# Optimization experiments

Hardware: AMD Instinct MI355X
Metric: run time of the kernel (lower is better)

The kernel has to match this reference:

```python
import jax, jax.numpy as jnp
import numpy as np

# D4 Daubechies filter taps (same filter replicated across all channels)
D4 = jnp.array([0.4829629131445341, 0.8365163037378079, 0.2241438680420134, -0.1294095225512604], dtype=jnp.float32)
N_SCALES = 11
SPARSE_DILATIONS = (512, 1024)


def setup_inputs() -> dict:
    key = jax.random.key(0)
    ks = jax.random.split(key, 12)
    B, N, D, H = 4, 4096, 1024, 16
    s = 0.02
    return {
        "x": jax.random.normal(ks[0], (B, N, D), dtype=jnp.float32),
        "Wqkv": jax.random.normal(ks[1], (D, 3 * D), dtype=jnp.float32) * s,
        "bqkv": jnp.zeros((3 * D,), dtype=jnp.float32),
        "Wout": jax.random.normal(ks[2], (D, D), dtype=jnp.float32) * s,
        "bout": jnp.zeros((D,), dtype=jnp.float32),
        "Wgate": jax.random.normal(ks[3], (D, D), dtype=jnp.float32) * s,
        "bgate": jnp.full((D,), 2.0, dtype=jnp.float32),  # nn.init.constant_(bias, 2.0)
        "scale_gain": jax.random.normal(ks[4], (N_SCALES, H), dtype=jnp.float32) * 0.1,
        "skip_w": jnp.full((len(SPARSE_DILATIONS),), -4.0, dtype=jnp.float32)
                  + jax.random.normal(ks[5], (len(SPARSE_DILATIONS),), dtype=jnp.float32) * 0.1,
        "coupling": jnp.eye(H, dtype=jnp.float32)
                    + 0.01 * jax.random.normal(ks[6], (H, H), dtype=jnp.float32),
    }


def _shift_right(t, s, N):
    """Causal shift along seq axis (axis=2): out[i] = t[i-s], zeros for i < s."""
    if s == 0:
        return t
    return jnp.pad(t, ((0, 0), (0, 0), (s, 0), (0, 0)))[:, :, :N, :]


def reference(x, Wqkv, bqkv, Wout, bout, Wgate, bgate, scale_gain, skip_w, coupling):
    B, N, D = x.shape
    H = scale_gain.shape[1]
    HD = D // H

    qkv = x @ Wqkv + bqkv                       # [B, N, 3D]
    q, k, v = jnp.split(qkv, 3, axis=-1)

    def to_heads(t):
        return t.reshape(B, N, H, HD).transpose(0, 2, 1, 3)  # [B, H, N, HD]

    q, k, v = to_heads(q), to_heads(k), to_heads(v)

    k_mag = jnp.linalg.norm(k, axis=-1, keepdims=True)       # [B, H, N, 1]
    field = v * k_mag                                        # [B, H, N, HD]

    # --- 11-scale causal D4 dilated depthwise conv pyramid ---
    # Depthwise conv with identical filter on every channel == weighted sum of
    # causally shifted copies: y[n] = sum_t D4[t] * field[n - (3-t)*d]
    gains = jax.nn.softmax(scale_gain, axis=0)               # [S, H]
    acc = jnp.zeros_like(field)
    for j in range(scale_gain.shape[0]):
        d = 1 << j
        y = sum(D4[t] * _shift_right(field, (3 - t) * d, N) for t in range(4))
        acc = acc + gains[j][None, :, None, None] * y
    field = acc

    # --- sparse long-distance causal skips (1-tap copies at d=512, 1024) ---
    sw = jax.nn.sigmoid(skip_w)
    skip = sum(sw[i] * _shift_right(field, d, N) for i, d in enumerate(SPARSE_DILATIONS))
    field = field + skip

    # --- gated field coupling across heads ---
    coup = jax.nn.softmax(coupling, axis=-1)                 # [H, H]
    field = jnp.einsum('ij,bjnd->bind', coup, field)

    q_flat = q.transpose(0, 2, 1, 3).reshape(B, N, D)
    gate = jax.nn.sigmoid(q_flat @ Wgate + bgate)
    gathered = field.transpose(0, 2, 1, 3).reshape(B, N, D)
    out = (gathered * gate) @ Wout + bout                    # dropout = identity (eval)
    return out
```

## Files before the change

### kernel.cpp

```cpp
#include <hip/hip_runtime.h>
#include <hip/hip_bf16.h>
#include <math.h>

#define BB 4
#define NSEQ 4096
#define DD 1024
#define HH 16
#define HD 64
#define MROWS (BB * NSEQ)

typedef __attribute__((ext_vector_type(8))) short short8;
typedef float v4f __attribute__((ext_vector_type(4)));
typedef unsigned short u16;

typedef __attribute__((address_space(1))) const void gconst_void;
typedef __attribute__((address_space(3))) void lds_void_t;

__device__ __constant__ int SHIFTS[24] = {0,1,2,3,4,6,8,12,16,24,32,48,64,96,128,192,256,384,512,768,1024,1536,2048,3072};

__device__ inline u16 f2bf(float f) {
    unsigned u = __float_as_uint(f);
    unsigned r = u + 0x7fffu + ((u >> 16) & 1u);
    return (u16)(r >> 16);
}
__device__ inline float bf2f(u16 h) {
    return __uint_as_float(((unsigned)h) << 16);
}
__device__ inline void gl2lds16(const u16* g, u16* l) {
    __builtin_amdgcn_global_load_lds((gconst_void*)g, (lds_void_t*)l, 16, 0, 0);
}

__device__ inline void tcast_dev(const float* __restrict__ W, long ldw, u16* __restrict__ WT, long ldt,
                                 int bx, int by, int tx, int ty, float (*tile)[33]) {
    long xg = (long)bx * 32 + tx;
    long y0 = (long)by * 32;
    for (int r = 0; r < 32; r += 8)
        tile[ty + r][tx] = W[(y0 + ty + r) * ldw + xg];
    __syncthreads();
    for (int r = 0; r < 32; r += 8)
        WT[((long)bx * 32 + ty + r) * ldt + y0 + tx] = f2bf(tile[tx][ty + r]);
}

__global__ __launch_bounds__(256) void prep_data_kernel(
    const float* __restrict__ x, const float* __restrict__ Wqkv,
    const float* __restrict__ Wgate, const float* __restrict__ Wout,
    const float* __restrict__ bqkv, const float* __restrict__ bgate,
    const float* __restrict__ scale_gain, const float* __restrict__ skip_w,
    const float* __restrict__ coupling,
    u16* __restrict__ xb, u16* __restrict__ WkvT, u16* __restrict__ WgateT,
    u16* __restrict__ WoutT, u16* __restrict__ WqC,
    float* __restrict__ bfuse, float* __restrict__ coefTab,
    float* __restrict__ coupS, float* __restrict__ swbuf) {
    __shared__ float tile[32][33];
    __shared__ float part[4][64];
    const int bid = blockIdx.x;
    const int t = threadIdx.x;
    const int tx = t & 31, ty = t >> 5;

    if (bid < 8192) {
        long i = ((long)bid * 256 + t) * 8;
        float4 f0 = *(const float4*)&x[i];
        float4 f1 = *(const float4*)&x[i + 4];
        u16 o[8];
        o[0] = f2bf(f0.x); o[1] = f2bf(f0.y); o[2] = f2bf(f0.z); o[3] = f2bf(f0.w);
        o[4] = f2bf(f1.x); o[5] = f2bf(f1.y); o[6] = f2bf(f1.z); o[7] = f2bf(f1.w);
        *(uint4*)&xb[i] = *(uint4*)o;
    } else if (bid < 10240) {
        int r = bid - 8192;
        tcast_dev(Wqkv + 1024, 3072, WkvT, 1024, r & 63, r >> 6, tx, ty, tile);
    } else if (bid < 11264) {
        int r = bid - 10240;
        tcast_dev(Wgate, 1024, WgateT, 1024, r & 31, r >> 5, tx, ty, tile);
    } else if (bid < 12288) {
        int r = bid - 11264;
        tcast_dev(Wout, 1024, WoutT, 1024, r & 31, r >> 5, tx, ty, tile);
    } else if (bid < 13312) {
        int r = bid - 12288;
        long i = ((long)r * 256 + t) * 4;
        int row = (int)(i >> 10);
        int col = (int)(i & 1023);
        float4 f = *(const float4*)&Wqkv[(long)row * 3072 + col];
        ushort4 o;
        o.x = f2bf(f.x); o.y = f2bf(f.y); o.z = f2bf(f.z); o.w = f2bf(f.w);
        *(ushort4*)&WqC[i] = o;
    } else if (bid < 13328) {
        int r = bid - 13312;
        int nloc = t & 63, strip = t >> 6;
        int n = r * 64 + nloc;
        float s = 0.f;
        for (int j = strip * 256; j < strip * 256 + 256; j++)
            s += bqkv[j] * Wgate[(long)j * 1024 + n];
        part[strip][nloc] = s;
        __syncthreads();
        if (strip == 0)
            bfuse[n] = bgate[n] + part[0][nloc] + part[1][nloc] + part[2][nloc] + part[3][nloc];
    } else {
        const float D4T[4] = {0.4829629131445341f, 0.8365163037378079f, 0.2241438680420134f, -0.1294095225512604f};
        if (t < 2) swbuf[t] = 1.0f / (1.0f + expf(-skip_w[t]));
        if (t < 16) {
            float m = -1e30f;
            for (int j = 0; j < 16; j++) m = fmaxf(m, coupling[t * 16 + j]);
            float s = 0.f, e[16];
            for (int j = 0; j < 16; j++) { e[j] = expf(coupling[t * 16 + j] - m); s += e[j]; }
            for (int j = 0; j < 16; j++) coupS[t * 16 + j] = e[j] / s;
            float g[11];
            m = -1e30f;
            for (int j = 0; j < 11; j++) m = fmaxf(m, scale_gain[j * 16 + t]);
            s = 0.f;
            for (int j = 0; j < 11; j++) { g[j] = expf(scale_gain[j * 16 + t] - m); s += g[j]; }
            for (int j = 0; j < 11; j++) g[j] /= s;
            float cf[24];
            for (int i = 0; i < 24; i++) cf[i] = 0.f;
            for (int j = 0; j < 11; j++) {
                int d = 1 << j;
                for (int tt = 0; tt < 4; tt++) {
                    int sh = (3 - tt) * d;
                    for (int i = 0; i < 24; i++) {
                        if (SHIFTS[i] == sh) { cf[i] += g[j] * D4T[tt]; break; }
                    }
                }
            }
            for (int i = 0; i < 24; i++) coefTab[t * 24 + i] = cf[i];
        }
    }
}

__global__ __launch_bounds__(256) void gemm64(const u16* __restrict__ A, long lda,
                                              const u16* __restrict__ BT, long ldb, int K,
                                              u16* __restrict__ C, long ldc) {
    __shared__ u16 As[64 * 32];
    __shared__ u16 Bs[64 * 32];
    const int tid = threadIdx.x;
    const int wv = tid >> 6, lane = tid & 63;
    const int wm = wv >> 1, wn = wv & 1;
    const int lrow = lane & 15, kq = lane >> 4;
    const long m0 = (long)blockIdx.y * 64, n0 = (long)blockIdx.x * 64;

    const int srow = wv * 16 + (lane >> 2);
    const int scol = ((lane & 3) ^ ((lane >> 3) & 3)) * 8;
    const u16* gA = A + (m0 + srow) * lda + scol;
    const u16* gB = BT + (n0 + srow) * ldb + scol;
    u16* la = &As[wv * 16 * 32];
    u16* lb = &Bs[wv * 16 * 32];

    const int acol = (kq ^ ((lrow >> 1) & 3)) * 8;
    v4f acc[2][2];
#pragma unroll
    for (int i = 0; i < 2; i++)
#pragma unroll
        for (int j = 0; j < 2; j++) acc[i][j] = (v4f){0.f, 0.f, 0.f, 0.f};

    for (int k0 = 0; k0 < K; k0 += 32) {
        gl2lds16(gA + k0, la);
        gl2lds16(gB + k0, lb);
        __syncthreads();
        short8 af[2], bf[2];
#pragma unroll
        for (int i = 0; i < 2; i++) af[i] = *(const short8*)&As[(wm * 32 + i * 16 + lrow) * 32 + acol];
#pragma unroll
        for (int j = 0; j < 2; j++) bf[j] = *(const short8*)&Bs[(wn * 32 + j * 16 + lrow) * 32 + acol];
#pragma unroll
        for (int im = 0; im < 2; im++)
#pragma unroll
            for (int in = 0; in < 2; in++)
                acc[im][in] = __builtin_amdgcn_mfma_f32_16x16x32_bf16(af[im], bf[in], acc[im][in], 0, 0, 0);
        __syncthreads();
    }
#pragma unroll
    for (int im = 0; im < 2; im++) {
#pragma unroll
        for (int in = 0; in < 2; in++) {
            long row = m0 + wm * 32 + im * 16 + kq * 4;
            long col = n0 + wn * 32 + in * 16 + lrow;
#pragma unroll
            for (int i = 0; i < 4; i++)
                C[(row + i) * ldc + col] = f2bf(acc[im][in][i]);
        }
    }
}

#define WAITV(N) asm volatile("s_waitcnt vmcnt(" #N ")" ::: "memory")

template <int CMODE>
__global__ __launch_bounds__(512, 2) void gemm256(const u16* __restrict__ A, long lda,
                                                  const u16* __restrict__ BT, long ldb, int K,
                                                  const float* __restrict__ bias,
                                                  const float* __restrict__ bias2,
                                                  void* __restrict__ C0, void* __restrict__ C1,
                                                  long ldc, float* __restrict__ kmagOut) {
    __shared__ u16 smem[4 * 2 * 8192];
    const int tid = threadIdx.x;
    const int wv = tid >> 6, lane = tid & 63;
    const int wm = wv >> 2, wn = wv & 3;
    const int lrow = lane & 15, kq = lane >> 4;

    const int nwg = gridDim.x * gridDim.y;
    const int lbid = blockIdx.y * gridDim.x + blockIdx.x;
    const int swz = (lbid & 7) * (nwg >> 3) + (lbid >> 3);
    const int bx = swz % gridDim.x, by = swz / gridDim.x;
    const long m0 = (long)by * 256, n0 = (long)bx * 256;

    const int srow = wv * 32 + (lane >> 2);
    const int scol = ((lane & 3) ^ ((lane >> 3) & 3)) * 8;
    const u16* gA0 = A + (m0 + srow) * lda + scol;
    const u16* gA1 = gA0 + 16 * lda;
    const u16* gB0 = BT + (n0 + srow) * ldb + scol;
    const u16* gB1 = gB0 + 16 * ldb;
    const int sb = wv * 32 * 32;

    const int acol = (kq ^ ((lrow >> 1) & 3)) * 8;
    const int aoff = (wm * 128 + lrow) * 32 + acol;
    const int boff = (wn * 64 + lrow) * 32 + acol;

    v4f acc[8][4];
#pragma unroll
    for (int i = 0; i < 8; i++)
#pragma unroll
        for (int j = 0; j < 4; j++) acc[i][j] = (v4f){0.f, 0.f, 0.f, 0.f};

    const int NT = K >> 5;

#define STAGE256(tt) {                                              \
        const int _kk = (tt) << 5;                                  \
        u16* _p = &smem[(((tt) & 3) * 2) * 8192 + sb];              \
        gl2lds16(gA0 + _kk, _p);                                    \
        gl2lds16(gA1 + _kk, _p + 512);                              \
        gl2lds16(gB0 + _kk, _p + 8192);                             \
        gl2lds16(gB1 + _kk, _p + 8192 + 512); }

    STAGE256(0)
    STAGE256(1)
    STAGE256(2)
    WAITV(8);
    __builtin_amdgcn_s_barrier();

    for (int t = 0; t < NT; ++t) {
        if (t + 3 < NT) STAGE256(t + 3)
        const u16* Ab = &smem[((t & 3) * 2) * 8192];
        const u16* Bb = Ab + 8192;
        short8 af[8], bf[4];
#pragma unroll
        for (int i = 0; i < 8; i++) af[i] = *(const short8*)&Ab[aoff + i * 512];
#pragma unroll
        for (int j = 0; j < 4; j++) bf[j] = *(const short8*)&Bb[boff + j * 512];
        __builtin_amdgcn_s_setprio(1);
#pragma unroll
        for (int i = 0; i < 8; i++)
#pragma unroll
            for (int j = 0; j < 4; j++)
                acc[i][j] = __builtin_amdgcn_mfma_f32_16x16x32_bf16(af[i], bf[j], acc[i][j], 0, 0, 0);
        __builtin_amdgcn_s_setprio(0);
        if (t + 3 < NT)      { WAITV(8); }
        else if (t + 2 < NT) { WAITV(4); }
        else if (t + 1 < NT) { WAITV(0); }
        __builtin_amdgcn_s_barrier();
    }
#undef STAGE256

    if (CMODE == 0) {
        float* C = (float*)C0;
#pragma unroll
        for (int im = 0; im < 8; im++) {
#pragma unroll
            for (int in = 0; in < 4; in++) {
                long row = m0 + wm * 128 + im * 16 + kq * 4;
                long col = n0 + wn * 64 + in * 16 + lrow;
                float bv = bias ? bias[col] : 0.f;
#pragma unroll
                for (int i = 0; i < 4; i++)
                    C[(row + i) * ldc + col] = acc[im][in][i] + bv;
            }
        }
    } else {
        u16* kvC = (u16*)C0;
        u16* gateC = (u16*)C1;
        const bool isGate = (n0 >= 2048);
        if (isGate) {
#pragma unroll
            for (int im = 0; im < 8; im++) {
#pragma unroll
                for (int in = 0; in < 4; in++) {
                    long row = m0 + wm * 128 + im * 16 + kq * 4;
                    long gc = n0 + wn * 64 + in * 16 + lrow - 2048;
                    float bv = bias2[gc];
#pragma unroll
                    for (int i = 0; i < 4; i++) {
                        float sgm = 1.0f / (1.0f + expf(-(acc[im][in][i] + bv)));
                        gateC[(row + i) * 1024 + gc] = f2bf(sgm);
                    }
                }
            }
        } else if (n0 < 1024) {
            float bvv[4];
#pragma unroll
            for (int in = 0; in < 4; in++) bvv[in] = bias[n0 + wn * 64 + in * 16 + lrow];
            const int h_g = (int)(n0 >> 6) + wn;
#pragma unroll
            for (int im = 0; im < 8; im++) {
                long row = m0 + wm * 128 + im * 16 + kq * 4;
                float ss0 = 0.f, ss1 = 0.f, ss2 = 0.f, ss3 = 0.f;
#pragma unroll
                for (int in = 0; in < 4; in++) {
                    long col = n0 + wn * 64 + in * 16 + lrow;
                    float v0 = acc[im][in][0] + bvv[in];
                    float v1 = acc[im][in][1] + bvv[in];
                    float v2 = acc[im][in][2] + bvv[in];
                    float v3 = acc[im][in][3] + bvv[in];
                    kvC[(row + 0) * 2048 + col] = f2bf(v0);
                    kvC[(row + 1) * 2048 + col] = f2bf(v1);
                    kvC[(row + 2) * 2048 + col] = f2bf(v2);
                    kvC[(row + 3) * 2048 + col] = f2bf(v3);
                    ss0 += v0 * v0; ss1 += v1 * v1; ss2 += v2 * v2; ss3 += v3 * v3;
                }
#pragma unroll
                for (int m = 1; m <= 8; m <<= 1) {
                    ss0 += __shfl_xor(ss0, m, 64);
                    ss1 += __shfl_xor(ss1, m, 64);
                    ss2 += __shfl_xor(ss2, m, 64);
                    ss3 += __shfl_xor(ss3, m, 64);
                }
                if (lrow == 0) {
                    int b = (int)(row >> 12);
                    int n = (int)(row & 4095);
                    float4 o4 = make_float4(sqrtf(ss0), sqrtf(ss1), sqrtf(ss2), sqrtf(ss3));
                    *(float4*)&kmagOut[((long)b * HH + h_g) * NSEQ + n] = o4;
                }
            }
        } else {
#pragma unroll
            for (int im = 0; im < 8; im++) {
#pragma unroll
                for (int in = 0; in < 4; in++) {
                    long row = m0 + wm * 128 + im * 16 + kq * 4;
                    long col = n0 + wn * 64 + in * 16 + lrow;
                    float bv = bias[col];
#pragma unroll
                    for (int i = 0; i < 4; i++)
                        kvC[(row + i) * 2048 + col] = f2bf(acc[im][in][i] + bv);
                }
            }
        }
    }
}

__global__ __launch_bounds__(256) void foldv_kernel(const u16* __restrict__ kv,
                                                    const float* __restrict__ kmag,
                                                    u16* __restrict__ field_t) {
    __shared__ u16 tile[64][72];
    int bh = blockIdx.y;
    int n0 = blockIdx.x * 64;
    int b = bh >> 4, h = bh & 15;
    int t = threadIdx.x;

    {
        int r = t >> 2;
        int c0 = (t & 3) * 16;
        int n = n0 + r;
        const u16* src = kv + ((long)(b * NSEQ + n)) * 2048 + 1024 + h * 64 + c0;
        uint4 u0 = *(const uint4*)src;
        uint4 u1 = *(const uint4*)(src + 8);
        float km = kmag[(long)bh * NSEQ + n];
        u16 in[16], o[16];
        *(uint4*)&in[0] = u0;
        *(uint4*)&in[8] = u1;
#pragma unroll
        for (int i = 0; i < 16; i++) o[i] = f2bf(bf2f(in[i]) * km);
        *(uint4*)&tile[r][c0] = *(uint4*)&o[0];
        *(uint4*)&tile[r][c0 + 8] = *(uint4*)&o[8];
    }
    __syncthreads();

    {
        int cg = t >> 4;
        int q = t & 15;
        u16 o[16];
#pragma unroll
        for (int j = 0; j < 4; j++) {
            int r = q * 4 + j;
            *(ushort4*)&o[j * 4] = *(const ushort4*)&tile[r][cg * 4];
        }
        u16* dst = field_t + (((long)bh * 16 + cg) * NSEQ + n0 + q * 4) * 4;
        *(uint4*)&dst[0] = *(uint4*)&o[0];
        *(uint4*)&dst[8] = *(uint4*)&o[8];
    }
}

__global__ __launch_bounds__(512) void pyramid_kernel(const u16* __restrict__ field_t,
                                                      const float* __restrict__ coefTab,
                                                      const float* __restrict__ swbuf,
                                                      u16* __restrict__ accp) {
    __shared__ u16 lds4[NSEQ * 4];
    int blk = blockIdx.x;
    int bh = blk >> 4;
    int cg = blk & 15;
    int hd0 = cg * 4;
    int h = bh & 15;
    int tid = threadIdx.x;

    float cf[24];
#pragma unroll
    for (int i = 0; i < 24; i++) cf[i] = coefTab[h * 24 + i];
    float sw0 = swbuf[0], sw1 = swbuf[1];

    const u16* src = field_t + ((long)bh * 16 + cg) * NSEQ * 4;
#pragma unroll
    for (int k = 0; k < 4; k++) {
        long e = ((long)k * 512 + tid) * 8;
        *(uint4*)&lds4[e] = *(const uint4*)&src[e];
    }
    __syncthreads();

    u16* dst = accp + (long)bh * NSEQ * HD + hd0;
    float p1x = 0.f, p1y = 0.f, p1z = 0.f, p1w = 0.f;
    float p2x = 0.f, p2y = 0.f, p2z = 0.f, p2w = 0.f;
    for (int i = 0; i < 8; i++) {
        int n = tid + i * 512;
        float ax = 0.f, ay = 0.f, az = 0.f, aw = 0.f;
#pragma unroll
        for (int tp = 0; tp < 24; tp++) {
            int s = SHIFTS[tp];
            if (n >= s) {
                const ushort4 f = *(const ushort4*)&lds4[(n - s) * 4];
                float c = cf[tp];
                ax += c * bf2f(f.x); ay += c * bf2f(f.y);
                az += c * bf2f(f.z); aw += c * bf2f(f.w);
            }
        }
        float ox = ax + sw0 * p1x + sw1 * p2x;
        float oy = ay + sw0 * p1y + sw1 * p2y;
        float oz = az + sw0 * p1z + sw1 * p2z;
        float ow = aw + sw0 * p1w + sw1 * p2w;
        ushort4 o;
        o.x = f2bf(ox); o.y = f2bf(oy); o.z = f2bf(oz); o.w = f2bf(ow);
        *(ushort4*)&dst[(long)n * HD] = o;
        p2x = p1x; p2y = p1y; p2z = p1z; p2w = p1w;
        p1x = ax;  p1y = ay;  p1z = az;  p1w = aw;
    }
}

__global__ __launch_bounds__(256) void couple_kernel(const u16* __restrict__ accp,
                                                     const u16* __restrict__ gate,
                                                     const float* __restrict__ coupS,
                                                     u16* __restrict__ A3) {
    __shared__ float tmp[DD];
    __shared__ float cp[256];
    int row = blockIdx.x;
    int b = row >> 12;
    int n = row & 4095;
    int tid = threadIdx.x;
    cp[tid] = coupS[tid];

    int e = tid * 4;
    int j = e >> 6;
    int hd = e & 63;
    const u16* base = accp + (((long)b * HH + j) * NSEQ + n) * HD + hd;
    ushort4 v0 = *(const ushort4*)base;
    tmp[e] = bf2f(v0.x); tmp[e + 1] = bf2f(v0.y);
    tmp[e + 2] = bf2f(v0.z); tmp[e + 3] = bf2f(v0.w);
    __syncthreads();

    float ox = 0.f, oy = 0.f, oz = 0.f, ow = 0.f;
#pragma unroll
    for (int jj = 0; jj < 16; jj++) {
        float c = cp[j * 16 + jj];
        ox += c * tmp[jj * 64 + hd];
        oy += c * tmp[jj * 64 + hd + 1];
        oz += c * tmp[jj * 64 + hd + 2];
        ow += c * tmp[jj * 64 + hd + 3];
    }
    const ushort4 g = *(const ushort4*)&gate[(long)row * DD + e];
    ox *= bf2f(g.x); oy *= bf2f(g.y); oz *= bf2f(g.z); ow *= bf2f(g.w);
    ushort4 o;
    o.x = f2bf(ox); o.y = f2bf(oy); o.z = f2bf(oz); o.w = f2bf(ow);
    *(ushort4*)&A3[(long)row * DD + e] = o;
}

extern "C" void kernel_launch(void* const* d_in, const int* in_sizes, int n_in,
                              void* d_out, int out_size, void* d_ws, size_t ws_size,
                              hipStream_t stream) {
    const float* x        = (const float*)d_in[0];
    const float* Wqkv     = (const float*)d_in[1];
    const float* bqkv     = (const float*)d_in[2];
    const float* Wout     = (const float*)d_in[3];
    const float* bout     = (const float*)d_in[4];
    const float* Wgate    = (const float*)d_in[5];
    const float* bgate    = (const float*)d_in[6];
    const float* scale_g  = (const float*)d_in[7];
    const float* skip_w   = (const float*)d_in[8];
    const float* coupling = (const float*)d_in[9];

    char* ws = (char*)d_ws;
    size_t off = 0;
    auto alloc = [&](size_t bytes) { char* p = ws + off; off += (bytes + 255) & ~(size_t)255; return p; };

    u16*   kv      = (u16*)alloc((size_t)MROWS * 2048 * 2);
    u16*   gate    = (u16*)alloc((size_t)MROWS * DD * 2);
    u16*   field_t = (u16*)alloc((size_t)BB * HH * NSEQ * HD * 2);
    u16*   WkvT    = (u16*)alloc((size_t)2048 * 1024 * 2);
    u16*   WfuseT  = (u16*)alloc((size_t)1024 * 1024 * 2);
    u16*   WgateT  = (u16*)alloc((size_t)1024 * 1024 * 2);
    u16*   WoutT   = (u16*)alloc((size_t)1024 * 1024 * 2);
    u16*   WqC     = (u16*)alloc((size_t)1024 * 1024 * 2);
    float* kmag    = (float*)alloc((size_t)BB * HH * NSEQ * 4);
    float* bfuse   = (float*)alloc(1024 * 4);
    float* coefT   = (float*)alloc(16 * 24 * 4);
    float* coupS   = (float*)alloc(256 * 4);
    float* swbuf   = (float*)alloc(2 * 4);
    u16*   xb   = field_t;
    u16*   accp = kv;
    u16*   A3   = kv + (size_t)BB * HH * NSEQ * HD;

    prep_data_kernel<<<13329, 256, 0, stream>>>(x, Wqkv, Wgate, Wout, bqkv, bgate,
                                                scale_g, skip_w, coupling,
                                                xb, WkvT, WgateT, WoutT, WqC,
                                                bfuse, coefT, coupS, swbuf);

    gemm64<<<dim3(16, 16), 256, 0, stream>>>(WgateT, 1024, WqC, 1024, 1024, WfuseT, 1024);

    gemm256<2><<<dim3(12, 64), 512, 0, stream>>>(xb, 1024, WkvT, 1024, 1024,
                                                 bqkv + 1024, bfuse, kv, gate, 0, kmag);

    foldv_kernel<<<dim3(64, 64), 256, 0, stream>>>(kv, kmag, field_t);

    pyramid_kernel<<<BB * HH * 16, 512, 0, stream>>>(field_t, coefT, swbuf, accp);

    couple_kernel<<<MROWS, 256, 0, stream>>>(accp, gate, coupS, A3);

    gemm256<0><<<dim3(4, 64), 512, 0, stream>>>(A3, 1024, WoutT, 1024, 1024,
                                                bout, (const float*)nullptr, (float*)d_out, nullptr,
                                                1024, (float*)nullptr);
}
```

Measured before the change: 432.3 us.

## Fuse V transpose into GEMM epilogue and k-norm scaling into pyramid load

```diff
diff --git a/kernel.cpp b/kernel.cpp
--- a/kernel.cpp
+++ b/kernel.cpp
@@ -272,7 +272,7 @@
             }
         }
     } else {
-        u16* kvC = (u16*)C0;
+        u16* fieldT = (u16*)C0;
         u16* gateC = (u16*)C1;
         const bool isGate = (n0 >= 2048);
         if (isGate) {
@@ -301,15 +301,10 @@
                 float ss0 = 0.f, ss1 = 0.f, ss2 = 0.f, ss3 = 0.f;
 #pragma unroll
                 for (int in = 0; in < 4; in++) {
-                    long col = n0 + wn * 64 + in * 16 + lrow;
                     float v0 = acc[im][in][0] + bvv[in];
                     float v1 = acc[im][in][1] + bvv[in];
                     float v2 = acc[im][in][2] + bvv[in];
                     float v3 = acc[im][in][3] + bvv[in];
-                    kvC[(row + 0) * 2048 + col] = f2bf(v0);
-                    kvC[(row + 1) * 2048 + col] = f2bf(v1);
-                    kvC[(row + 2) * 2048 + col] = f2bf(v2);
-                    kvC[(row + 3) * 2048 + col] = f2bf(v3);
                     ss0 += v0 * v0; ss1 += v1 * v1; ss2 += v2 * v2; ss3 += v3 * v3;
                 }
 #pragma unroll
@@ -327,65 +322,29 @@
                 }
             }
         } else {
+            const int vc0 = (int)(n0 - 1024);
 #pragma unroll
             for (int im = 0; im < 8; im++) {
 #pragma unroll
                 for (int in = 0; in < 4; in++) {
                     long row = m0 + wm * 128 + im * 16 + kq * 4;
-                    long col = n0 + wn * 64 + in * 16 + lrow;
-                    float bv = bias[col];
+                    int vcol = vc0 + wn * 64 + in * 16 + lrow;
+                    float bv = bias[1024 + vcol];
+                    int b = (int)(row >> 12);
+                    int nn = (int)(row & 4095);
+                    int h = vcol >> 6, hd = vcol & 63;
+                    u16* dstb = fieldT + (((long)(b * 16 + h) * 16 + (hd >> 2)) * NSEQ + nn) * 4 + (hd & 3);
 #pragma unroll
                     for (int i = 0; i < 4; i++)
-                        kvC[(row + i) * 2048 + col] = f2bf(acc[im][in][i] + bv);
+                        dstb[(long)i * 4] = f2bf(acc[im][in][i] + bv);
                 }
             }
         }
     }
 }
 
-__global__ __launch_bounds__(256) void foldv_kernel(const u16* __restrict__ kv,
-                                                    const float* __restrict__ kmag,
-                                                    u16* __restrict__ field_t) {
-    __shared__ u16 tile[64][72];
-    int bh = blockIdx.y;
-    int n0 = blockIdx.x * 64;
-    int b = bh >> 4, h = bh & 15;
-    int t = threadIdx.x;
-
-    {
-        int r = t >> 2;
-        int c0 = (t & 3) * 16;
-        int n = n0 + r;
-        const u16* src = kv + ((long)(b * NSEQ + n)) * 2048 + 1024 + h * 64 + c0;
-        uint4 u0 = *(const uint4*)src;
-        uint4 u1 = *(const uint4*)(src + 8);
-        float km = kmag[(long)bh * NSEQ + n];
-        u16 in[16], o[16];
-        *(uint4*)&in[0] = u0;
-        *(uint4*)&in[8] = u1;
-#pragma unroll
-        for (int i = 0; i < 16; i++) o[i] = f2bf(bf2f(in[i]) * km);
-        *(uint4*)&tile[r][c0] = *(uint4*)&o[0];
-        *(uint4*)&tile[r][c0 + 8] = *(uint4*)&o[8];
-    }
-    __syncthreads();
-
-    {
-        int cg = t >> 4;
-        int q = t & 15;
-        u16 o[16];
-#pragma unroll
-        for (int j = 0; j < 4; j++) {
-            int r = q * 4 + j;
-            *(ushort4*)&o[j * 4] = *(const ushort4*)&tile[r][cg * 4];
-        }
-        u16* dst = field_t + (((long)bh * 16 + cg) * NSEQ + n0 + q * 4) * 4;
-        *(uint4*)&dst[0] = *(uint4*)&o[0];
-        *(uint4*)&dst[8] = *(uint4*)&o[8];
-    }
-}
-
 __global__ __launch_bounds__(512) void pyramid_kernel(const u16* __restrict__ field_t,
+                                                      const float* __restrict__ kmag,
                                                       const float* __restrict__ coefTab,
                                                       const float* __restrict__ swbuf,
                                                       u16* __restrict__ accp) {
@@ -403,10 +362,20 @@
     float sw0 = swbuf[0], sw1 = swbuf[1];
 
     const u16* src = field_t + ((long)bh * 16 + cg) * NSEQ * 4;
+    const float* kmb = kmag + (long)bh * NSEQ;
 #pragma unroll
     for (int k = 0; k < 4; k++) {
         long e = ((long)k * 512 + tid) * 8;
-        *(uint4*)&lds4[e] = *(const uint4*)&src[e];
+        uint4 raw = *(const uint4*)&src[e];
+        int np = (int)(e >> 2);
+        float2 km = *(const float2*)&kmb[np];
+        u16 in8[8], o8[8];
+        *(uint4*)in8 = raw;
+#pragma unroll
+        for (int q = 0; q < 4; q++) o8[q] = f2bf(bf2f(in8[q]) * km.x);
+#pragma unroll
+        for (int q = 4; q < 8; q++) o8[q] = f2bf(bf2f(in8[q]) * km.y);
+        *(uint4*)&lds4[e] = *(uint4*)o8;
     }
     __syncthreads();
 
@@ -493,9 +462,9 @@
     size_t off = 0;
     auto alloc = [&](size_t bytes) { char* p = ws + off; off += (bytes + 255) & ~(size_t)255; return p; };
 
-    u16*   kv      = (u16*)alloc((size_t)MROWS * 2048 * 2);
+    u16*   kvreg   = (u16*)alloc((size_t)MROWS * 2048 * 2);
     u16*   gate    = (u16*)alloc((size_t)MROWS * DD * 2);
-    u16*   field_t = (u16*)alloc((size_t)BB * HH * NSEQ * HD * 2);
+    u16*   reg1    = (u16*)alloc((size_t)BB * HH * NSEQ * HD * 2);
     u16*   WkvT    = (u16*)alloc((size_t)2048 * 1024 * 2);
     u16*   WfuseT  = (u16*)alloc((size_t)1024 * 1024 * 2);
     u16*   WgateT  = (u16*)alloc((size_t)1024 * 1024 * 2);
@@ -506,9 +475,10 @@
     float* coefT   = (float*)alloc(16 * 24 * 4);
     float* coupS   = (float*)alloc(256 * 4);
     float* swbuf   = (float*)alloc(2 * 4);
-    u16*   xb   = field_t;
-    u16*   accp = kv;
-    u16*   A3   = kv + (size_t)BB * HH * NSEQ * HD;
+    u16*   fieldT = kvreg;
+    u16*   A3     = kvreg + (size_t)BB * HH * NSEQ * HD;
+    u16*   xb     = reg1;
+    u16*   accp   = reg1;
 
     prep_data_kernel<<<13329, 256, 0, stream>>>(x, Wqkv, Wgate, Wout, bqkv, bgate,
                                                 scale_g, skip_w, coupling,
@@ -518,11 +488,9 @@
     gemm64<<<dim3(16, 16), 256, 0, stream>>>(WgateT, 1024, WqC, 1024, 1024, WfuseT, 1024);
 
     gemm256<2><<<dim3(12, 64), 512, 0, stream>>>(xb, 1024, WkvT, 1024, 1024,
-                                                 bqkv + 1024, bfuse, kv, gate, 0, kmag);
-
-    foldv_kernel<<<dim3(64, 64), 256, 0, stream>>>(kv, kmag, field_t);
-
-    pyramid_kernel<<<BB * HH * 16, 512, 0, stream>>>(field_t, coefT, swbuf, accp);
+                                                 bqkv + 1024, bfuse, fieldT, gate, 0, kmag);
+
+    pyramid_kernel<<<BB * HH * 16, 512, 0, stream>>>(fieldT, kmag, coefT, swbuf, accp);
 
     couple_kernel<<<MROWS, 256, 0, stream>>>(accp, gate, coupS, A3);
 
```

Result: faster. 405.8 us (-6.1%).
